# Kernel optimization log

Hardware: AMD Instinct MI355X
Metric: run time of the kernel (lower is better)

## Reference

```python
import jax, jax.numpy as jnp
import numpy as np


def setup_inputs() -> dict:
    key = jax.random.key(0)
    k1, k2, k3, k4 = jax.random.split(key, 4)
    B, S, IN, OUT = 4, 2048, 4096, 4096
    x = jax.random.normal(k1, (B, S, IN), dtype=jnp.float32)
    # 4-bit signed range [-8, 7], stored widened (torch uses int8)
    weight_quantized = jax.random.randint(k2, (OUT, IN), -8, 8, dtype=jnp.int32)
    # per-output-row scale, positive and small (abs-max / 7 style)
    weight_scale = jax.random.uniform(k3, (OUT,), dtype=jnp.float32) * 0.01 + 1e-4
    bias = jax.random.normal(k4, (OUT,), dtype=jnp.float32) * 0.01
    return {"x": x, "weight_quantized": weight_quantized,
            "weight_scale": weight_scale, "bias": bias}


def reference(x, weight_quantized, weight_scale, bias):
    # dequantize: [OUT, IN] int -> fp32 scaled per output row
    w = weight_quantized.astype(jnp.float32) * weight_scale[:, None]
    # F.linear: x @ w.T + bias  -> [B, S, OUT]
    out = jnp.einsum('bsi,oi->bso', x, w) + bias
    return out
```

## Files before the change

kernel.cpp:

```cpp
#include <hip/hip_runtime.h>
#include <hip/hip_bf16.h>

typedef __bf16 bf16x4 __attribute__((ext_vector_type(4)));
typedef __bf16 bf16x8 __attribute__((ext_vector_type(8)));
typedef float  floatx4 __attribute__((ext_vector_type(4)));

#define AS1 __attribute__((address_space(1)))
#define AS3 __attribute__((address_space(3)))

#define BM2 256
#define BN2 256
#define BK2 64

#define BARRIER() asm volatile("s_barrier" ::: "memory")

__global__ __launch_bounds__(256)
void cvt_both8(const float* __restrict__ xin, const int* __restrict__ win,
               __bf16* __restrict__ xout, __bf16* __restrict__ wout,
               int nx8, int nw8)
{
    const int stride = gridDim.x * 256;
    const int total  = nx8 + nw8;
    for (int i = blockIdx.x * 256 + threadIdx.x; i < total; i += stride) {
        if (i < nx8) {
            const float4* p = reinterpret_cast<const float4*>(xin) + (size_t)i * 2;
            float4 a = p[0], b = p[1];
            bf16x8 h;
            h[0] = (__bf16)a.x; h[1] = (__bf16)a.y; h[2] = (__bf16)a.z; h[3] = (__bf16)a.w;
            h[4] = (__bf16)b.x; h[5] = (__bf16)b.y; h[6] = (__bf16)b.z; h[7] = (__bf16)b.w;
            reinterpret_cast<bf16x8*>(xout)[i] = h;
        } else {
            int j = i - nx8;
            const int4* p = reinterpret_cast<const int4*>(win) + (size_t)j * 2;
            int4 a = p[0], b = p[1];
            bf16x8 h;
            h[0] = (__bf16)(float)a.x; h[1] = (__bf16)(float)a.y;
            h[2] = (__bf16)(float)a.z; h[3] = (__bf16)(float)a.w;
            h[4] = (__bf16)(float)b.x; h[5] = (__bf16)(float)b.y;
            h[6] = (__bf16)(float)b.z; h[7] = (__bf16)(float)b.w;
            reinterpret_cast<bf16x8*>(wout)[j] = h;
        }
    }
}

template<int P>
__device__ __forceinline__ void mfma_cluster(floatx4 (&acc)[8][4],
                                             const bf16x8 (&af)[2][2],
                                             const bf16x8 (&bfr)[4][2])
{
    __builtin_amdgcn_s_setprio(1);
#pragma unroll
    for (int h = 0; h < 2; ++h)
#pragma unroll
        for (int ii = 0; ii < 2; ++ii)
#pragma unroll
            for (int j = 0; j < 4; ++j)
                acc[2 * P + ii][j] = __builtin_amdgcn_mfma_f32_16x16x32_bf16(
                    af[ii][h], bfr[j][h], acc[2 * P + ii][j], 0, 0, 0);
    __builtin_amdgcn_s_setprio(0);
}

__device__ __forceinline__ void read_af(bf16x8 (&dst)[2][2], const __bf16* cA,
                                        int rowBase, int lm, int kq, int sw)
{
#pragma unroll
    for (int ii = 0; ii < 2; ++ii)
#pragma unroll
        for (int h = 0; h < 2; ++h)
            dst[ii][h] = *reinterpret_cast<const bf16x8*>(
                &cA[(rowBase + ii * 16 + lm) * BK2 + ((kq + h * 4) ^ sw) * 8]);
}

__device__ __forceinline__ void read_bf(bf16x8 (&dst)[4][2], const __bf16* cB,
                                        int wn, int lm, int kq, int sw)
{
#pragma unroll
    for (int j = 0; j < 4; ++j)
#pragma unroll
        for (int h = 0; h < 2; ++h)
            dst[j][h] = *reinterpret_cast<const bf16x8*>(
                &cB[(wn + j * 16 + lm) * BK2 + ((kq + h * 4) ^ sw) * 8]);
}

__global__ __launch_bounds__(512)
void gemm_bf16_bt_pipe(const __bf16* __restrict__ A, const __bf16* __restrict__ B,
                       const float* __restrict__ scale, const float* __restrict__ bias,
                       float* __restrict__ Out, int M, int N, int K)
{
    __shared__ __bf16 sA[2][BM2 * BK2];
    __shared__ __bf16 sB[2][BN2 * BK2];

    const int tid  = threadIdx.x;
    const int wave = tid >> 6;
    const int lane = tid & 63;
    const int row0 = blockIdx.y * BM2;
    const int col0 = blockIdx.x * BN2;

    const int sRow = lane >> 3;
    const int gBlk = (lane & 7) ^ sRow;
    const size_t aBase = (size_t)(row0 + wave * 8 + sRow) * K + gBlk * 8;
    const size_t bBase = (size_t)(col0 + wave * 8 + sRow) * K + gBlk * 8;
    const int ldsWOff = wave * 8 * BK2;

#define STAGE_A(buf, q, kt_) \
    __builtin_amdgcn_global_load_lds( \
        (const AS1 void*)(A + aBase + (size_t)(q) * 64 * K + (size_t)(kt_) * BK2), \
        (AS3 void*)&sA[(buf)][(q) * 64 * BK2 + ldsWOff], 16, 0, 0)
#define STAGE_B(buf, q, kt_) \
    __builtin_amdgcn_global_load_lds( \
        (const AS1 void*)(B + bBase + (size_t)(q) * 64 * K + (size_t)(kt_) * BK2), \
        (AS3 void*)&sB[(buf)][(q) * 64 * BK2 + ldsWOff], 16, 0, 0)

    const int wm = (wave >> 2) * 128;
    const int wn = (wave & 3) * 64;
    const int lm = lane & 15;
    const int kq = lane >> 4;
    const int sw = lm & 7;

    floatx4 acc[8][4];
#pragma unroll
    for (int i = 0; i < 8; ++i)
#pragma unroll
        for (int j = 0; j < 4; ++j)
            acc[i][j] = (floatx4)0.0f;

    bf16x8 bfr[4][2];
    bf16x8 afE[2][2];
    bf16x8 afO[2][2];
    const int nt = K / BK2;

    STAGE_A(0, 0, 0); STAGE_A(0, 2, 0);
    STAGE_B(0, 0, 0); STAGE_B(0, 1, 0); STAGE_B(0, 2, 0); STAGE_B(0, 3, 0);
    STAGE_A(0, 1, 0); STAGE_A(0, 3, 0);
    STAGE_B(1, 0, 1); STAGE_B(1, 1, 1); STAGE_B(1, 2, 1); STAGE_B(1, 3, 1);
    STAGE_A(1, 0, 1); STAGE_A(1, 2, 1);
    asm volatile("s_waitcnt vmcnt(8)" ::: "memory");
    BARRIER();
    read_bf(bfr, sB[0], wn, lm, kq, sw);
    read_af(afE, sA[0], wm, lm, kq, sw);

#define TILE(c, n1, n2)                                                        \
                                                                       \
    STAGE_A((c) ^ 1, 1, n1); STAGE_A((c) ^ 1, 3, n1);                          \
    read_af(afO, sA[(c)], wm + 32, lm, kq, sw);                                \
    mfma_cluster<0>(acc, afE, bfr);                                            \
    asm volatile("s_waitcnt vmcnt(8)" ::: "memory");                           \
    BARRIER();                                                                 \
                                                                       \
    STAGE_B((c), 0, n2); STAGE_B((c), 1, n2);                                  \
    STAGE_B((c), 2, n2); STAGE_B((c), 3, n2);                                  \
    read_af(afE, sA[(c)], wm + 64, lm, kq, sw);                                \
    mfma_cluster<1>(acc, afO, bfr);                                            \
    BARRIER();                                                                 \
                                                                       \
    STAGE_A((c), 0, n2); STAGE_A((c), 2, n2);                                  \
    read_af(afO, sA[(c)], wm + 96, lm, kq, sw);                                \
    mfma_cluster<2>(acc, afE, bfr);                                            \
    asm volatile("s_waitcnt vmcnt(8)" ::: "memory");                           \
    BARRIER();                                                                 \
                                                                       \
    read_af(afE, sA[(c) ^ 1], wm, lm, kq, sw);                                 \
    mfma_cluster<3>(acc, afO, bfr);                                            \
    read_bf(bfr, sB[(c) ^ 1], wn, lm, kq, sw);                                 \
    BARRIER();

    for (int it = 0; it < nt / 2; ++it) {
        const int kt = 2 * it;
        const int e1 = kt + 1;
        const int e2 = (kt + 2 < nt) ? kt + 2 : 0;
        const int o2 = (kt + 3 < nt) ? kt + 3 : 0;
        TILE(0, e1, e2)
        TILE(1, e2, o2)
    }
    asm volatile("s_waitcnt vmcnt(0)" ::: "memory");
#undef TILE
#undef STAGE_A
#undef STAGE_B

#pragma unroll
    for (int j = 0; j < 4; ++j) {
        int n = col0 + wn + j * 16 + lm;
        float sc = scale[n];
        float bi = bias[n];
#pragma unroll
        for (int i = 0; i < 8; ++i) {
#pragma unroll
            for (int r = 0; r < 4; ++r) {
                int m = row0 + wm + i * 16 + kq * 4 + r;
                Out[(size_t)m * N + n] = sc * acc[i][j][r] + bi;
            }
        }
    }
}

#define BM 128
#define BN 128

__global__ __launch_bounds__(256)
void fp4linear_gemm(const float* __restrict__ X, const int* __restrict__ W,
                    const float* __restrict__ scale, const float* __restrict__ bias,
                    float* __restrict__ Out, int M, int N, int K)
{
    __shared__ __bf16 sA[BM * 32];
    __shared__ __bf16 sB[BN * 32];

    const int tid  = threadIdx.x;
    const int row0 = blockIdx.y * BM;
    const int col0 = blockIdx.x * BN;
    const int wave = tid >> 6;
    const int lane = tid & 63;
    const int wm = (wave >> 1) * 64;
    const int wn = (wave & 1) * 64;
    const int lm = lane & 15;
    const int kq = lane >> 4;

    floatx4 acc[4][4];
#pragma unroll
    for (int i = 0; i < 4; ++i)
#pragma unroll
        for (int j = 0; j < 4; ++j)
            acc[i][j] = (floatx4)0.0f;

    for (int k0 = 0; k0 < K; k0 += 32) {
        float4 fa[4];
        int4   ib[4];
#pragma unroll
        for (int l = 0; l < 4; ++l) {
            int idx = tid + l * 256;
            int r = idx >> 3, c4 = idx & 7;
            fa[l] = *reinterpret_cast<const float4*>(
                        &X[(size_t)(row0 + r) * K + k0 + c4 * 4]);
        }
#pragma unroll
        for (int l = 0; l < 4; ++l) {
            int idx = tid + l * 256;
            int r = idx >> 3, c4 = idx & 7;
            ib[l] = *reinterpret_cast<const int4*>(
                        &W[(size_t)(col0 + r) * K + k0 + c4 * 4]);
        }
        __syncthreads();
#pragma unroll
        for (int l = 0; l < 4; ++l) {
            int idx = tid + l * 256;
            int r = idx >> 3, c4 = idx & 7;
            bf16x4 h;
            h[0] = (__bf16)fa[l].x; h[1] = (__bf16)fa[l].y;
            h[2] = (__bf16)fa[l].z; h[3] = (__bf16)fa[l].w;
            *reinterpret_cast<bf16x4*>(&sA[r * 32 + c4 * 4]) = h;
        }
#pragma unroll
        for (int l = 0; l < 4; ++l) {
            int idx = tid + l * 256;
            int r = idx >> 3, c4 = idx & 7;
            bf16x4 h;
            h[0] = (__bf16)(float)ib[l].x; h[1] = (__bf16)(float)ib[l].y;
            h[2] = (__bf16)(float)ib[l].z; h[3] = (__bf16)(float)ib[l].w;
            *reinterpret_cast<bf16x4*>(&sB[r * 32 + c4 * 4]) = h;
        }
        __syncthreads();

        bf16x8 af[4], bfr[4];
#pragma unroll
        for (int i = 0; i < 4; ++i)
            af[i] = *reinterpret_cast<const bf16x8*>(
                        &sA[(wm + i * 16 + lm) * 32 + kq * 8]);
#pragma unroll
        for (int j = 0; j < 4; ++j)
            bfr[j] = *reinterpret_cast<const bf16x8*>(
                        &sB[(wn + j * 16 + lm) * 32 + kq * 8]);
#pragma unroll
        for (int i = 0; i < 4; ++i)
#pragma unroll
            for (int j = 0; j < 4; ++j)
                acc[i][j] = __builtin_amdgcn_mfma_f32_16x16x32_bf16(
                                af[i], bfr[j], acc[i][j], 0, 0, 0);
    }

#pragma unroll
    for (int j = 0; j < 4; ++j) {
        int n = col0 + wn + j * 16 + lm;
        float sc = scale[n];
        float bi = bias[n];
#pragma unroll
        for (int i = 0; i < 4; ++i) {
#pragma unroll
            for (int r = 0; r < 4; ++r) {
                int m = row0 + wm + i * 16 + kq * 4 + r;
                Out[(size_t)m * N + n] = sc * acc[i][j][r] + bi;
            }
        }
    }
}

extern "C" void kernel_launch(void* const* d_in, const int* in_sizes, int n_in,
                              void* d_out, int out_size, void* d_ws, size_t ws_size,
                              hipStream_t stream) {
    const float* x     = (const float*)d_in[0];
    const int*   wq    = (const int*)d_in[1];
    const float* scale = (const float*)d_in[2];
    const float* bias  = (const float*)d_in[3];
    float* out = (float*)d_out;

    const int N = in_sizes[2];
    const int K = in_sizes[1] / N;
    const int M = in_sizes[0] / K;

    const size_t xElems = (size_t)M * K;
    const size_t wElems = (size_t)N * K;
    const size_t need   = (xElems + wElems) * sizeof(__bf16);

    const bool cvt_ok = (ws_size >= need) && (xElems % 8 == 0) && (wElems % 8 == 0);
    const int  nt     = K / BK2;
    const bool gemm_ok = (M % BM2 == 0) && (N % BN2 == 0) && (K % BK2 == 0) &&
                         (nt % 2 == 0) && (nt >= 4);

    if (cvt_ok && gemm_ok) {
        __bf16* xb = (__bf16*)d_ws;
        __bf16* wb = xb + xElems;
        int nx8 = (int)(xElems / 8);
        int nw8 = (int)(wElems / 8);
        int total = nx8 + nw8;
        int cvtBlocks = (total + 255) / 256;
        if (cvtBlocks > 2048) cvtBlocks = 2048;
        hipLaunchKernelGGL(cvt_both8, dim3(cvtBlocks), dim3(256), 0, stream,
                           x, wq, xb, wb, nx8, nw8);
        hipLaunchKernelGGL(gemm_bf16_bt_pipe, dim3(N / BN2, M / BM2), dim3(512),
                           0, stream, xb, wb, scale, bias, out, M, N, K);
        return;
    }

    hipLaunchKernelGGL(fp4linear_gemm, dim3(N / BN, M / BM), dim3(256), 0, stream,
                       x, wq, scale, bias, out, M, N, K);
}
```

Before: 530.3 us.

## Restructure bf16 GEMM main loop into eight-phase pipeline with half-tile LDS staging

Replaces the four-phase-per-tile software pipeline with an eight-phase schedule. LDS A and B tiles are split into 128-row halves, and each phase stages one half-tile of the next K slice while running 16 MFMAs on the current one. Each phase is fenced with sched_barriers and s_barriers, and the waitcnt is placed only every fourth phase. The aim is finer-grained overlap of global-to-LDS loads with MFMA work. In exchange it adds twice as many barriers per tile and drops the register double-buffering of A fragments, so LDS reads are no longer overlapped with the previous cluster.

Result: faster. 508.5 us (-4.1%).

```diff
diff --git a/kernel.cpp b/kernel.cpp
--- a/kernel.cpp
+++ b/kernel.cpp
@@ -11,6 +11,8 @@
 #define BM2 256
 #define BN2 256
 #define BK2 64
+#define HALF (128 * 64)
+#define ABUF (2 * HALF)
 
 #define BARRIER() asm volatile("s_barrier" ::: "memory")
 
@@ -43,52 +45,50 @@
     }
 }
 
-template<int P>
-__device__ __forceinline__ void mfma_cluster(floatx4 (&acc)[8][4],
-                                             const bf16x8 (&af)[2][2],
-                                             const bf16x8 (&bfr)[4][2])
-{
-    __builtin_amdgcn_s_setprio(1);
+template<int Q>
+__device__ __forceinline__ void mfma16(floatx4 (&acc)[8][4],
+                                       const bf16x8 (&af)[2][2],
+                                       const bf16x8 (&bfr)[4][2])
+{
 #pragma unroll
     for (int h = 0; h < 2; ++h)
 #pragma unroll
         for (int ii = 0; ii < 2; ++ii)
 #pragma unroll
             for (int j = 0; j < 4; ++j)
-                acc[2 * P + ii][j] = __builtin_amdgcn_mfma_f32_16x16x32_bf16(
-                    af[ii][h], bfr[j][h], acc[2 * P + ii][j], 0, 0, 0);
-    __builtin_amdgcn_s_setprio(0);
-}
-
-__device__ __forceinline__ void read_af(bf16x8 (&dst)[2][2], const __bf16* cA,
-                                        int rowBase, int lm, int kq, int sw)
+                acc[2 * Q + ii][j] = __builtin_amdgcn_mfma_f32_16x16x32_bf16(
+                    af[ii][h], bfr[j][h], acc[2 * Q + ii][j], 0, 0, 0);
+}
+
+__device__ __forceinline__ void read_afH(bf16x8 (&dst)[2][2], const __bf16* p,
+                                         int rowBase, int lm, int kq, int sw)
 {
 #pragma unroll
     for (int ii = 0; ii < 2; ++ii)
 #pragma unroll
         for (int h = 0; h < 2; ++h)
             dst[ii][h] = *reinterpret_cast<const bf16x8*>(
-                &cA[(rowBase + ii * 16 + lm) * BK2 + ((kq + h * 4) ^ sw) * 8]);
-}
-
-__device__ __forceinline__ void read_bf(bf16x8 (&dst)[4][2], const __bf16* cB,
-                                        int wn, int lm, int kq, int sw)
+                &p[(rowBase + ii * 16 + lm) * 64 + ((kq + h * 4) ^ sw) * 8]);
+}
+
+__device__ __forceinline__ void read_bfH(bf16x8 (&dst)[4][2], const __bf16* p,
+                                         int wnh, int lm, int kq, int sw)
 {
 #pragma unroll
     for (int j = 0; j < 4; ++j)
 #pragma unroll
         for (int h = 0; h < 2; ++h)
             dst[j][h] = *reinterpret_cast<const bf16x8*>(
-                &cB[(wn + j * 16 + lm) * BK2 + ((kq + h * 4) ^ sw) * 8]);
+                &p[(wnh + j * 16 + lm) * 64 + ((kq + h * 4) ^ sw) * 8]);
 }
 
 __global__ __launch_bounds__(512)
-void gemm_bf16_bt_pipe(const __bf16* __restrict__ A, const __bf16* __restrict__ B,
-                       const float* __restrict__ scale, const float* __restrict__ bias,
-                       float* __restrict__ Out, int M, int N, int K)
-{
-    __shared__ __bf16 sA[2][BM2 * BK2];
-    __shared__ __bf16 sB[2][BN2 * BK2];
+void gemm_bf16_bt_8ph(const __bf16* __restrict__ A, const __bf16* __restrict__ B,
+                      const float* __restrict__ scale, const float* __restrict__ bias,
+                      float* __restrict__ Out, int M, int N, int K)
+{
+    __shared__ __bf16 sA[2 * ABUF];
+    __shared__ __bf16 sB[2 * ABUF];
 
     const int tid  = threadIdx.x;
     const int wave = tid >> 6;
@@ -100,22 +100,28 @@
     const int gBlk = (lane & 7) ^ sRow;
     const size_t aBase = (size_t)(row0 + wave * 8 + sRow) * K + gBlk * 8;
     const size_t bBase = (size_t)(col0 + wave * 8 + sRow) * K + gBlk * 8;
-    const int ldsWOff = wave * 8 * BK2;
-
-#define STAGE_A(buf, q, kt_) \
+    const int dOff = wave * 8 * 64;
+
+#define STG_A(buf, h, sub, kt_) \
     __builtin_amdgcn_global_load_lds( \
-        (const AS1 void*)(A + aBase + (size_t)(q) * 64 * K + (size_t)(kt_) * BK2), \
-        (AS3 void*)&sA[(buf)][(q) * 64 * BK2 + ldsWOff], 16, 0, 0)
-#define STAGE_B(buf, q, kt_) \
+        (const AS1 void*)(A + aBase + (size_t)((h) * 128 + (sub) * 64) * K + (size_t)(kt_) * BK2), \
+        (AS3 void*)(sA + (buf) * ABUF + (h) * HALF + (sub) * 64 * 64 + dOff), 16, 0, 0)
+#define STG_B(buf, h, sub, kt_) \
     __builtin_amdgcn_global_load_lds( \
-        (const AS1 void*)(B + bBase + (size_t)(q) * 64 * K + (size_t)(kt_) * BK2), \
-        (AS3 void*)&sB[(buf)][(q) * 64 * BK2 + ldsWOff], 16, 0, 0)
-
-    const int wm = (wave >> 2) * 128;
-    const int wn = (wave & 3) * 64;
-    const int lm = lane & 15;
-    const int kq = lane >> 4;
-    const int sw = lm & 7;
+        (const AS1 void*)(B + bBase + (size_t)((h) * 128 + (sub) * 64) * K + (size_t)(kt_) * BK2), \
+        (AS3 void*)(sB + (buf) * ABUF + (h) * HALF + (sub) * 64 * 64 + dOff), 16, 0, 0)
+#define STGH_A(buf, h, kt_) do { STG_A(buf, h, 0, kt_); STG_A(buf, h, 1, kt_); } while (0)
+#define STGH_B(buf, h, kt_) do { STG_B(buf, h, 0, kt_); STG_B(buf, h, 1, kt_); } while (0)
+
+    const int hA  = wave >> 2;
+    const int hB  = (wave & 3) >> 1;
+    const int wnh = (wave & 1) * 64;
+    const int lm  = lane & 15;
+    const int kq  = lane >> 4;
+    const int sw  = lm & 7;
+
+    const __bf16* aH[2] = { sA + hA * HALF, sA + ABUF + hA * HALF };
+    const __bf16* bH[2] = { sB + hB * HALF, sB + ABUF + hB * HALF };
 
     floatx4 acc[8][4];
 #pragma unroll
@@ -125,58 +131,54 @@
             acc[i][j] = (floatx4)0.0f;
 
     bf16x8 bfr[4][2];
-    bf16x8 afE[2][2];
-    bf16x8 afO[2][2];
+    bf16x8 af[2][2];
     const int nt = K / BK2;
 
-    STAGE_A(0, 0, 0); STAGE_A(0, 2, 0);
-    STAGE_B(0, 0, 0); STAGE_B(0, 1, 0); STAGE_B(0, 2, 0); STAGE_B(0, 3, 0);
-    STAGE_A(0, 1, 0); STAGE_A(0, 3, 0);
-    STAGE_B(1, 0, 1); STAGE_B(1, 1, 1); STAGE_B(1, 2, 1); STAGE_B(1, 3, 1);
-    STAGE_A(1, 0, 1); STAGE_A(1, 2, 1);
-    asm volatile("s_waitcnt vmcnt(8)" ::: "memory");
+    STGH_B(0, 0, 0); STGH_B(0, 1, 0);
+    STGH_A(0, 0, 0); STGH_A(0, 1, 0);
+    STGH_B(1, 0, 1); STGH_B(1, 1, 1);
+    asm volatile("s_waitcnt vmcnt(4)" ::: "memory");
     BARRIER();
-    read_bf(bfr, sB[0], wn, lm, kq, sw);
-    read_af(afE, sA[0], wm, lm, kq, sw);
-
-#define TILE(c, n1, n2)                                                        \
-                                                                       \
-    STAGE_A((c) ^ 1, 1, n1); STAGE_A((c) ^ 1, 3, n1);                          \
-    read_af(afO, sA[(c)], wm + 32, lm, kq, sw);                                \
-    mfma_cluster<0>(acc, afE, bfr);                                            \
-    asm volatile("s_waitcnt vmcnt(8)" ::: "memory");                           \
-    BARRIER();                                                                 \
-                                                                       \
-    STAGE_B((c), 0, n2); STAGE_B((c), 1, n2);                                  \
-    STAGE_B((c), 2, n2); STAGE_B((c), 3, n2);                                  \
-    read_af(afE, sA[(c)], wm + 64, lm, kq, sw);                                \
-    mfma_cluster<1>(acc, afO, bfr);                                            \
-    BARRIER();                                                                 \
-                                                                       \
-    STAGE_A((c), 0, n2); STAGE_A((c), 2, n2);                                  \
-    read_af(afO, sA[(c)], wm + 96, lm, kq, sw);                                \
-    mfma_cluster<2>(acc, afE, bfr);                                            \
-    asm volatile("s_waitcnt vmcnt(8)" ::: "memory");                           \
-    BARRIER();                                                                 \
-                                                                       \
-    read_af(afE, sA[(c) ^ 1], wm, lm, kq, sw);                                 \
-    mfma_cluster<3>(acc, afO, bfr);                                            \
-    read_bf(bfr, sB[(c) ^ 1], wn, lm, kq, sw);                                 \
-    BARRIER();
+
+#define PH(Q, c, DOB, STAGE, DOVM)                                             \
+    do {                                                                       \
+        if (DOB) read_bfH(bfr, bH[c], wnh, lm, kq, sw);                        \
+        read_afH(af, aH[c], (Q) * 32, lm, kq, sw);                             \
+        STAGE;                                                                 \
+        BARRIER();                                                             \
+        __builtin_amdgcn_sched_barrier(0);                                     \
+        __builtin_amdgcn_s_setprio(1);                                         \
+        mfma16<Q>(acc, af, bfr);                                               \
+        __builtin_amdgcn_s_setprio(0);                                         \
+        __builtin_amdgcn_sched_barrier(0);                                     \
+        if (DOVM) asm volatile("s_waitcnt vmcnt(4)" ::: "memory");             \
+        BARRIER();                                                             \
+    } while (0)
 
     for (int it = 0; it < nt / 2; ++it) {
         const int kt = 2 * it;
         const int e1 = kt + 1;
         const int e2 = (kt + 2 < nt) ? kt + 2 : 0;
-        const int o2 = (kt + 3 < nt) ? kt + 3 : 0;
-        TILE(0, e1, e2)
-        TILE(1, e2, o2)
+        const int e3 = (kt + 3 < nt) ? kt + 3 : 0;
+
+        PH(0, 0, true,  STGH_A(1, 0, e1), false);
+        PH(1, 0, false, STGH_A(1, 1, e1), false);
+        PH(2, 0, false, STGH_B(0, 0, e2), false);
+        PH(3, 0, false, STGH_B(0, 1, e2), true );
+        PH(0, 1, true,  STGH_A(0, 0, e2), false);
+        PH(1, 1, false, STGH_A(0, 1, e2), false);
+        PH(2, 1, false, STGH_B(1, 0, e3), false);
+        PH(3, 1, false, STGH_B(1, 1, e3), true );
     }
     asm volatile("s_waitcnt vmcnt(0)" ::: "memory");
-#undef TILE
-#undef STAGE_A
-#undef STAGE_B
-
+#undef PH
+#undef STGH_A
+#undef STGH_B
+#undef STG_A
+#undef STG_B
+
+    const int wm = hA * 128;
+    const int wn = (wave & 3) * 64;
 #pragma unroll
     for (int j = 0; j < 4; ++j) {
         int n = col0 + wn + j * 16 + lm;
@@ -324,7 +326,7 @@
         if (cvtBlocks > 2048) cvtBlocks = 2048;
         hipLaunchKernelGGL(cvt_both8, dim3(cvtBlocks), dim3(256), 0, stream,
                            x, wq, xb, wb, nx8, nw8);
-        hipLaunchKernelGGL(gemm_bf16_bt_pipe, dim3(N / BN2, M / BM2), dim3(512),
+        hipLaunchKernelGGL(gemm_bf16_bt_8ph, dim3(N / BN2, M / BM2), dim3(512),
                            0, stream, xb, wb, scale, bias, out, M, N, K);
         return;
     }
```
